# Performance work log

Measured on AMD Instinct MI355X. Metric: run time of the kernel, lower is better.

Reference implementation:

```python
import jax, jax.numpy as jnp
import numpy as np

K = 1024  # number of superpixel ids (matches fill_max of superpixel)

@jax.custom_vjp
def smooth_square(x):
    return x * x

def _ss_fwd(x):
    return x * x, x

def _ss_bwd(x, g):
    # gradient of square with input clipped to [-1, 1]
    return (g * 2.0 * jnp.clip(x, -1.0, 1.0),)

smooth_square.defvjp(_ss_fwd, _ss_bwd)

def setup_inputs() -> dict:
    key = jax.random.key(0)
    k1, k2 = jax.random.split(key)
    D, H, W = 64, 1024, 1024
    embedding = jax.random.normal(k1, (D, H, W), dtype=jnp.float32)
    superpixel = jax.random.randint(k2, (H, W), 0, K, dtype=jnp.int64)
    return {"embedding": embedding, "superpixel": superpixel}

def reference(embedding, superpixel):
    # embedding: D x H x W float, superpixel: H x W int
    D = embedding.shape[0]
    sp = superpixel.reshape(-1)                      # N = H*W
    x = embedding.reshape(D, -1)                     # D x N
    ones = jnp.ones(sp.shape, dtype=x.dtype)
    counts = jax.ops.segment_sum(ones, sp, num_segments=K)        # K
    sums = jax.ops.segment_sum(x.T, sp, num_segments=K)           # K x D
    mean = sums / jnp.maximum(counts, 1.0)[:, None]                # K x D
    dev = x - mean[sp].T                              # D x N, scores - per-segment mean
    # sum over all segments of D*variance*count == sum of squared deviations
    return smooth_square(dev).sum()
```

## Files before the change

kernel.cpp:

```cpp
#include <hip/hip_runtime.h>
#include <stdint.h>

#define K_SEG 1024
#define D_CH 64
#define CHUNK 32768
#define ABLK 512
#define PREP_B 128


__global__ void __launch_bounds__(256)
prep_kernel(const int* __restrict__ spw, uint16_t* __restrict__ sp16,
            uint32_t* __restrict__ cnt_part, float* __restrict__ sums,
            uint32_t* __restrict__ ticket, int N) {
    __shared__ uint32_t h[4][K_SEG];
    __shared__ int wideflag;
    const int t = threadIdx.x;
    const int b = blockIdx.x;
    {
        uint32_t* hf = &h[0][0];
        for (int i = t; i < 4 * K_SEG; i += 256) hf[i] = 0u;
    }
    if (t < 64) {
        int odd = spw[2 * t + 1];
        unsigned long long bal = __ballot(odd == 0);
        if (t == 0) wideflag = (bal == ~0ULL) ? 1 : 0;
    }
    if (b == 0 && t == 0) *ticket = 0u;
    if (b < D_CH)
        for (int i = t; i < K_SEG; i += 256) sums[b * K_SEG + i] = 0.0f;
    __syncthreads();
    const bool wide = (wideflag != 0);
    uint32_t* ht = h[t >> 6];
    const int stride = PREP_B * 256;
    #pragma unroll 4
    for (int n = b * 256 + t; n < N; n += stride) {
        int v = wide ? spw[2 * n] : spw[n];
        v &= (K_SEG - 1);
        sp16[n] = (uint16_t)v;
        ht[v] += 1u;
    }
    __syncthreads();
    for (int k = t; k < K_SEG; k += 256)
        cnt_part[b * K_SEG + k] = h[0][k] + h[1][k] + h[2][k] + h[3][k];
}

__global__ void __launch_bounds__(ABLK, 8)
accum_kernel(const float* __restrict__ emb, const uint16_t* __restrict__ sp16,
             float* __restrict__ sums, double* __restrict__ xsq_part, int N) {
    __shared__ float2 lsum[4][K_SEG];
    __shared__ float wsum[8];
    const int t = threadIdx.x;
    float2* tile = lsum[(t >> 6) & 3];
    {
        float2* lf = &lsum[0][0];
        for (int i = t; i < 4 * K_SEG; i += ABLK) lf[i] = make_float2(0.0f, 0.0f);
    }
    __syncthreads();

    const int g = blockIdx.x;
    const int c = blockIdx.y;
    const int base = c * CHUNK;
    const float* e0 = emb + (size_t)(2 * g) * N + base;
    const float* e1 = e0 + N;
    const uint16_t* sp = sp16 + base;
    float acc = 0.0f;
    const int NIT = CHUNK / (ABLK * 4);

    if (base + CHUNK <= N) {
        int q = t * 4;
        ushort4 k4 = *reinterpret_cast<const ushort4*>(sp + q);
        float4 v0 = *reinterpret_cast<const float4*>(e0 + q);
        float4 v1 = *reinterpret_cast<const float4*>(e1 + q);
        #pragma unroll 2
        for (int it = 0; it < NIT; ++it) {
            const int qn = q + ABLK * 4;
            ushort4 k4n = k4; float4 v0n = v0, v1n = v1;
            if (it + 1 < NIT) {
                k4n = *reinterpret_cast<const ushort4*>(sp + qn);
                v0n = *reinterpret_cast<const float4*>(e0 + qn);
                v1n = *reinterpret_cast<const float4*>(e1 + qn);
            }
            acc += v0.x * v0.x + v0.y * v0.y + v0.z * v0.z + v0.w * v0.w;
            acc += v1.x * v1.x + v1.y * v1.y + v1.z * v1.z + v1.w * v1.w;
            float2 o;
            o = tile[k4.x]; o.x += v0.x; o.y += v1.x; tile[k4.x] = o;
            o = tile[k4.y]; o.x += v0.y; o.y += v1.y; tile[k4.y] = o;
            o = tile[k4.z]; o.x += v0.z; o.y += v1.z; tile[k4.z] = o;
            o = tile[k4.w]; o.x += v0.w; o.y += v1.w; tile[k4.w] = o;
            q = qn; k4 = k4n; v0 = v0n; v1 = v1n;
        }
    } else {
        for (int it = 0; it < NIT; ++it) {
            const int p = base + it * ABLK * 4 + t * 4;
            if (p + 4 <= N) {
                const ushort4 k4 = *reinterpret_cast<const ushort4*>(sp16 + p);
                const float4 v0 = *reinterpret_cast<const float4*>(emb + (size_t)(2 * g) * N + p);
                const float4 v1 = *reinterpret_cast<const float4*>(emb + (size_t)(2 * g + 1) * N + p);
                acc += v0.x * v0.x + v0.y * v0.y + v0.z * v0.z + v0.w * v0.w;
                acc += v1.x * v1.x + v1.y * v1.y + v1.z * v1.z + v1.w * v1.w;
                float2 o;
                o = tile[k4.x]; o.x += v0.x; o.y += v1.x; tile[k4.x] = o;
                o = tile[k4.y]; o.x += v0.y; o.y += v1.y; tile[k4.y] = o;
                o = tile[k4.z]; o.x += v0.z; o.y += v1.z; tile[k4.z] = o;
                o = tile[k4.w]; o.x += v0.w; o.y += v1.w; tile[k4.w] = o;
            }
        }
    }
    __syncthreads();

    for (int k = t; k < K_SEG; k += ABLK) {
        float2 s0 = lsum[0][k], s1 = lsum[1][k], s2 = lsum[2][k], s3 = lsum[3][k];
        atomicAdd(&sums[(size_t)(2 * g) * K_SEG + k], s0.x + s1.x + s2.x + s3.x);
        atomicAdd(&sums[(size_t)(2 * g + 1) * K_SEG + k], s0.y + s1.y + s2.y + s3.y);
    }

    #pragma unroll
    for (int off = 32; off; off >>= 1) acc += __shfl_down(acc, off, 64);
    if ((t & 63) == 0) wsum[t >> 6] = acc;
    __syncthreads();
    if (t == 0) {
        double bsum = 0.0;
        #pragma unroll
        for (int w = 0; w < 8; ++w) bsum += (double)wsum[w];
        xsq_part[c * gridDim.x + g] = bsum;
    }
}

__global__ void __launch_bounds__(256)
finalize_kernel(const float* __restrict__ sums, const uint32_t* __restrict__ cnt_part,
                const double* __restrict__ xsq_part, double* __restrict__ term_part,
                uint32_t* __restrict__ ticket, float* __restrict__ out,
                int n_xsq) {
    const int t = threadIdx.x;
    const int b = blockIdx.x;
    const int k0 = b * 16;
    __shared__ float cinv[16];
    if (t < 16) {
        uint32_t c = 0;
        #pragma unroll 8
        for (int p = 0; p < PREP_B; ++p) c += cnt_part[p * K_SEG + k0 + t];
        cinv[t] = 1.0f / fmaxf((float)c, 1.0f);
    }
    __syncthreads();
    double acc = 0.0;
    for (int e = t; e < D_CH * 16; e += 256) {
        const int d = e >> 4, kk = e & 15;
        const float s = sums[d * K_SEG + k0 + kk];
        acc += (double)(s * s) * (double)cinv[kk];
    }
    __shared__ double sacc[256];
    sacc[t] = acc;
    __syncthreads();
    for (int off = 128; off; off >>= 1) {
        if (t < off) sacc[t] += sacc[t + off];
        __syncthreads();
    }
    __shared__ int last;
    if (t == 0) {
        term_part[b] = sacc[0];
        __threadfence();
        last = (atomicAdd(ticket, 1u) == gridDim.x - 1) ? 1 : 0;
    }
    __syncthreads();
    if (last) {
        double a = 0.0;
        for (int i = t; i < n_xsq; i += 256) a += xsq_part[i];
        if (t < 64) a -= atomicAdd(&term_part[t], 0.0);
        sacc[t] = a;
        __syncthreads();
        for (int off = 128; off; off >>= 1) {
            if (t < off) sacc[t] += sacc[t + off];
            __syncthreads();
        }
        if (t == 0) out[0] = (float)sacc[0];
    }
}

extern "C" void kernel_launch(void* const* d_in, const int* in_sizes, int n_in,
                              void* d_out, int out_size, void* d_ws, size_t ws_size,
                              hipStream_t stream) {
    const float* emb = (const float*)d_in[0];
    const int* spw = (const int*)d_in[1];
    const int N = in_sizes[1];

    char* ws = (char*)d_ws;
    uint32_t* ticket = (uint32_t*)(ws + 0);
    double* term_part = (double*)(ws + 64);
    double* xsq_part = (double*)(ws + 1024);
    float* sums = (float*)(ws + 16384);
    uint32_t* cnt_part = (uint32_t*)(ws + 278528);
    uint16_t* sp16 = (uint16_t*)(ws + 802816);

    prep_kernel<<<PREP_B, 256, 0, stream>>>(spw, sp16, cnt_part, sums, ticket, N);

    dim3 grid(D_CH / 2, (N + CHUNK - 1) / CHUNK);
    accum_kernel<<<grid, ABLK, 0, stream>>>(emb, sp16, sums, xsq_part, N);

    const int n_xsq = grid.x * grid.y;
    finalize_kernel<<<64, 256, 0, stream>>>(sums, cnt_part, xsq_part, term_part,
                                            ticket, (float*)d_out, n_xsq);
}
```

Measured before the change: 68.61 us.

## Replace global atomic segment sums with per-chunk partials and vectorized prep

When workspace allows, accum blocks write per-chunk partial sums to distinct slots instead of issuing global atomicAdds. A finalize kernel then reduces those partials over chunks per (d,k). The count reduction and reciprocal move into the g==0 accum blocks, and prep now uses 256 blocks of 512 threads with int4 loads and ushort4 stores. Atomic contention goes away, at the cost of extra partial-buffer traffic (32x64x1024 floats) and a serial chunk loop in finalize.

```diff
diff --git a/kernel.cpp b/kernel.cpp
--- a/kernel.cpp
+++ b/kernel.cpp
@@ -5,20 +5,22 @@
 #define D_CH 64
 #define CHUNK 32768
 #define ABLK 512
-#define PREP_B 128
-
-
-__global__ void __launch_bounds__(256)
-prep_kernel(const int* __restrict__ spw, uint16_t* __restrict__ sp16,
-            uint32_t* __restrict__ cnt_part, float* __restrict__ sums,
-            uint32_t* __restrict__ ticket, int N) {
-    __shared__ uint32_t h[4][K_SEG];
+#define NPREP_A 256
+#define TPREP_A 512
+#define NPREP_B 128
+#define TPREP_B 256
+
+
+__global__ void prep_kernel(const int* __restrict__ spw, uint16_t* __restrict__ sp16,
+                            uint32_t* __restrict__ cnt_part, float* __restrict__ sums,
+                            uint32_t* __restrict__ ticket, int N, int zero_sums) {
+    __shared__ uint32_t h[8][K_SEG];
     __shared__ int wideflag;
-    const int t = threadIdx.x;
-    const int b = blockIdx.x;
+    const int t = threadIdx.x, b = blockIdx.x;
+    const int tpb = blockDim.x, nw = tpb >> 6;
     {
         uint32_t* hf = &h[0][0];
-        for (int i = t; i < 4 * K_SEG; i += 256) hf[i] = 0u;
+        for (int i = t; i < nw * K_SEG; i += tpb) hf[i] = 0u;
     }
     if (t < 64) {
         int odd = spw[2 * t + 1];
@@ -26,29 +28,47 @@
         if (t == 0) wideflag = (bal == ~0ULL) ? 1 : 0;
     }
     if (b == 0 && t == 0) *ticket = 0u;
-    if (b < D_CH)
-        for (int i = t; i < K_SEG; i += 256) sums[b * K_SEG + i] = 0.0f;
+    if (zero_sums) {
+        for (int i = t; i < (D_CH * K_SEG) / NPREP_B; i += tpb)
+            sums[b * ((D_CH * K_SEG) / NPREP_B) + i] = 0.0f;
+    }
     __syncthreads();
     const bool wide = (wideflag != 0);
     uint32_t* ht = h[t >> 6];
-    const int stride = PREP_B * 256;
-    #pragma unroll 4
-    for (int n = b * 256 + t; n < N; n += stride) {
-        int v = wide ? spw[2 * n] : spw[n];
-        v &= (K_SEG - 1);
-        sp16[n] = (uint16_t)v;
-        ht[v] += 1u;
-    }
-    __syncthreads();
-    for (int k = t; k < K_SEG; k += 256)
-        cnt_part[b * K_SEG + k] = h[0][k] + h[1][k] + h[2][k] + h[3][k];
-}
-
+    const int step = gridDim.x * tpb * 4;
+    for (int n0 = (b * tpb + t) * 4; n0 + 4 <= N; n0 += step) {
+        int i0, i1, i2, i3;
+        if (wide) {
+            int4 a = *reinterpret_cast<const int4*>(spw + 2 * (size_t)n0);
+            int4 c = *reinterpret_cast<const int4*>(spw + 2 * (size_t)n0 + 4);
+            i0 = a.x; i1 = a.z; i2 = c.x; i3 = c.z;
+        } else {
+            int4 a = *reinterpret_cast<const int4*>(spw + n0);
+            i0 = a.x; i1 = a.y; i2 = a.z; i3 = a.w;
+        }
+        i0 &= K_SEG - 1; i1 &= K_SEG - 1; i2 &= K_SEG - 1; i3 &= K_SEG - 1;
+        ushort4 s4;
+        s4.x = (uint16_t)i0; s4.y = (uint16_t)i1; s4.z = (uint16_t)i2; s4.w = (uint16_t)i3;
+        *reinterpret_cast<ushort4*>(sp16 + n0) = s4;
+        ht[i0]++; ht[i1]++; ht[i2]++; ht[i3]++;
+    }
+    __syncthreads();
+    for (int k = t; k < K_SEG; k += tpb) {
+        uint32_t c = 0;
+        for (int w = 0; w < nw; ++w) c += h[w][k];
+        cnt_part[(size_t)b * K_SEG + k] = c;
+    }
+}
+
+template <bool PARTIALS>
 __global__ void __launch_bounds__(ABLK, 8)
 accum_kernel(const float* __restrict__ emb, const uint16_t* __restrict__ sp16,
-             float* __restrict__ sums, double* __restrict__ xsq_part, int N) {
+             float* __restrict__ outp, float* __restrict__ cinv,
+             const uint32_t* __restrict__ cnt_part, double* __restrict__ xsq_part,
+             int N, int nchunks) {
     __shared__ float2 lsum[4][K_SEG];
     __shared__ float wsum[8];
+    __shared__ int lastdummy;  (void)lastdummy;
     const int t = threadIdx.x;
     float2* tile = lsum[(t >> 6) & 3];
     {
@@ -82,11 +102,18 @@
             }
             acc += v0.x * v0.x + v0.y * v0.y + v0.z * v0.z + v0.w * v0.w;
             acc += v1.x * v1.x + v1.y * v1.y + v1.z * v1.z + v1.w * v1.w;
-            float2 o;
-            o = tile[k4.x]; o.x += v0.x; o.y += v1.x; tile[k4.x] = o;
-            o = tile[k4.y]; o.x += v0.y; o.y += v1.y; tile[k4.y] = o;
-            o = tile[k4.z]; o.x += v0.z; o.y += v1.z; tile[k4.z] = o;
-            o = tile[k4.w]; o.x += v0.w; o.y += v1.w; tile[k4.w] = o;
+            float2 o0 = tile[k4.x];
+            float2 o1 = tile[k4.y];
+            float2 o2 = tile[k4.z];
+            float2 o3 = tile[k4.w];
+            o0.x += v0.x; o0.y += v1.x;
+            o1.x += v0.y; o1.y += v1.y;
+            o2.x += v0.z; o2.y += v1.z;
+            o3.x += v0.w; o3.y += v1.w;
+            tile[k4.x] = o0;
+            tile[k4.y] = o1;
+            tile[k4.z] = o2;
+            tile[k4.w] = o3;
             q = qn; k4 = k4n; v0 = v0n; v1 = v1n;
         }
     } else {
@@ -98,20 +125,29 @@
                 const float4 v1 = *reinterpret_cast<const float4*>(emb + (size_t)(2 * g + 1) * N + p);
                 acc += v0.x * v0.x + v0.y * v0.y + v0.z * v0.z + v0.w * v0.w;
                 acc += v1.x * v1.x + v1.y * v1.y + v1.z * v1.z + v1.w * v1.w;
-                float2 o;
-                o = tile[k4.x]; o.x += v0.x; o.y += v1.x; tile[k4.x] = o;
-                o = tile[k4.y]; o.x += v0.y; o.y += v1.y; tile[k4.y] = o;
-                o = tile[k4.z]; o.x += v0.z; o.y += v1.z; tile[k4.z] = o;
-                o = tile[k4.w]; o.x += v0.w; o.y += v1.w; tile[k4.w] = o;
+                float2 o0 = tile[k4.x], o1 = tile[k4.y], o2 = tile[k4.z], o3 = tile[k4.w];
+                o0.x += v0.x; o0.y += v1.x;
+                o1.x += v0.y; o1.y += v1.y;
+                o2.x += v0.z; o2.y += v1.z;
+                o3.x += v0.w; o3.y += v1.w;
+                tile[k4.x] = o0; tile[k4.y] = o1; tile[k4.z] = o2; tile[k4.w] = o3;
             }
         }
     }
     __syncthreads();
 
+    const size_t baseA = ((size_t)c * D_CH + 2 * g) * K_SEG;
     for (int k = t; k < K_SEG; k += ABLK) {
         float2 s0 = lsum[0][k], s1 = lsum[1][k], s2 = lsum[2][k], s3 = lsum[3][k];
-        atomicAdd(&sums[(size_t)(2 * g) * K_SEG + k], s0.x + s1.x + s2.x + s3.x);
-        atomicAdd(&sums[(size_t)(2 * g + 1) * K_SEG + k], s0.y + s1.y + s2.y + s3.y);
+        float sx = s0.x + s1.x + s2.x + s3.x;
+        float sy = s0.y + s1.y + s2.y + s3.y;
+        if (PARTIALS) {
+            outp[baseA + k] = sx;
+            outp[baseA + K_SEG + k] = sy;
+        } else {
+            atomicAdd(&outp[(size_t)(2 * g) * K_SEG + k], sx);
+            atomicAdd(&outp[(size_t)(2 * g + 1) * K_SEG + k], sy);
+        }
     }
 
     #pragma unroll
@@ -124,30 +160,41 @@
         for (int w = 0; w < 8; ++w) bsum += (double)wsum[w];
         xsq_part[c * gridDim.x + g] = bsum;
     }
+
+    if (PARTIALS && g == 0) {
+        __syncthreads();
+        uint32_t* sc = reinterpret_cast<uint32_t*>(&lsum[0][0]);
+        for (int kbase = c * 32; kbase < K_SEG; kbase += 32 * nchunks) {
+            const int kk = kbase + (t & 31);
+            uint32_t s = 0;
+            const int j0 = (t >> 5) * (NPREP_A / 16);
+            for (int j = j0; j < j0 + NPREP_A / 16; ++j)
+                s += cnt_part[(size_t)j * K_SEG + kk];
+            sc[(t >> 5) * 32 + (t & 31)] = s;
+            __syncthreads();
+            if (t < 32) {
+                uint32_t ctot = 0;
+                #pragma unroll
+                for (int sl = 0; sl < 16; ++sl) ctot += sc[sl * 32 + t];
+                cinv[kbase + t] = 1.0f / fmaxf((float)ctot, 1.0f);
+            }
+            __syncthreads();
+        }
+    }
 }
 
 __global__ void __launch_bounds__(256)
-finalize_kernel(const float* __restrict__ sums, const uint32_t* __restrict__ cnt_part,
-                const double* __restrict__ xsq_part, double* __restrict__ term_part,
-                uint32_t* __restrict__ ticket, float* __restrict__ out,
-                int n_xsq) {
-    const int t = threadIdx.x;
-    const int b = blockIdx.x;
-    const int k0 = b * 16;
-    __shared__ float cinv[16];
-    if (t < 16) {
-        uint32_t c = 0;
-        #pragma unroll 8
-        for (int p = 0; p < PREP_B; ++p) c += cnt_part[p * K_SEG + k0 + t];
-        cinv[t] = 1.0f / fmaxf((float)c, 1.0f);
-    }
-    __syncthreads();
-    double acc = 0.0;
-    for (int e = t; e < D_CH * 16; e += 256) {
-        const int d = e >> 4, kk = e & 15;
-        const float s = sums[d * K_SEG + k0 + kk];
-        acc += (double)(s * s) * (double)cinv[kk];
-    }
+finalizeA_kernel(const float* __restrict__ part, const float* __restrict__ cinv,
+                 double* __restrict__ xsq_part, double* __restrict__ term_part,
+                 uint32_t* __restrict__ ticket, float* __restrict__ out,
+                 int nchunks, int n_xsq) {
+    const int t = threadIdx.x, b = blockIdx.x;
+    const int d = b >> 2;
+    const int k = (b & 3) * 256 + t;
+    float S = 0.0f;
+    for (int c = 0; c < nchunks; ++c)
+        S += part[((size_t)c * D_CH + d) * K_SEG + k];
+    double acc = (double)S * (double)S * (double)cinv[k];
     __shared__ double sacc[256];
     sacc[t] = acc;
     __syncthreads();
@@ -164,7 +211,55 @@
     __syncthreads();
     if (last) {
         double a = 0.0;
-        for (int i = t; i < n_xsq; i += 256) a += xsq_part[i];
+        for (int i = t; i < n_xsq; i += 256) a += atomicAdd(&xsq_part[i], 0.0);
+        a -= atomicAdd(&term_part[t], 0.0);
+        sacc[t] = a;
+        __syncthreads();
+        for (int off = 128; off; off >>= 1) {
+            if (t < off) sacc[t] += sacc[t + off];
+            __syncthreads();
+        }
+        if (t == 0) out[0] = (float)sacc[0];
+    }
+}
+
+__global__ void __launch_bounds__(256)
+finalizeB_kernel(const float* __restrict__ sums, const uint32_t* __restrict__ cnt_part,
+                 double* __restrict__ xsq_part, double* __restrict__ term_part,
+                 uint32_t* __restrict__ ticket, float* __restrict__ out, int n_xsq) {
+    const int t = threadIdx.x, b = blockIdx.x;
+    const int k0 = b * 16;
+    __shared__ float cinv16[16];
+    if (t < 16) {
+        uint32_t c = 0;
+        #pragma unroll 8
+        for (int p = 0; p < NPREP_B; ++p) c += cnt_part[p * K_SEG + k0 + t];
+        cinv16[t] = 1.0f / fmaxf((float)c, 1.0f);
+    }
+    __syncthreads();
+    double acc = 0.0;
+    for (int e = t; e < D_CH * 16; e += 256) {
+        const int d = e >> 4, kk = e & 15;
+        const float s = sums[d * K_SEG + k0 + kk];
+        acc += (double)(s * s) * (double)cinv16[kk];
+    }
+    __shared__ double sacc[256];
+    sacc[t] = acc;
+    __syncthreads();
+    for (int off = 128; off; off >>= 1) {
+        if (t < off) sacc[t] += sacc[t + off];
+        __syncthreads();
+    }
+    __shared__ int last;
+    if (t == 0) {
+        term_part[b] = sacc[0];
+        __threadfence();
+        last = (atomicAdd(ticket, 1u) == gridDim.x - 1) ? 1 : 0;
+    }
+    __syncthreads();
+    if (last) {
+        double a = 0.0;
+        for (int i = t; i < n_xsq; i += 256) a += atomicAdd(&xsq_part[i], 0.0);
         if (t < 64) a -= atomicAdd(&term_part[t], 0.0);
         sacc[t] = a;
         __syncthreads();
@@ -182,21 +277,42 @@
     const float* emb = (const float*)d_in[0];
     const int* spw = (const int*)d_in[1];
     const int N = in_sizes[1];
+    const int nchunks = (N + CHUNK - 1) / CHUNK;
 
     char* ws = (char*)d_ws;
     uint32_t* ticket = (uint32_t*)(ws + 0);
     double* term_part = (double*)(ws + 64);
-    double* xsq_part = (double*)(ws + 1024);
-    float* sums = (float*)(ws + 16384);
-    uint32_t* cnt_part = (uint32_t*)(ws + 278528);
-    uint16_t* sp16 = (uint16_t*)(ws + 802816);
-
-    prep_kernel<<<PREP_B, 256, 0, stream>>>(spw, sp16, cnt_part, sums, ticket, N);
-
-    dim3 grid(D_CH / 2, (N + CHUNK - 1) / CHUNK);
-    accum_kernel<<<grid, ABLK, 0, stream>>>(emb, sp16, sums, xsq_part, N);
-
-    const int n_xsq = grid.x * grid.y;
-    finalize_kernel<<<64, 256, 0, stream>>>(sums, cnt_part, xsq_part, term_part,
-                                            ticket, (float*)d_out, n_xsq);
-}
+    double* xsq_part = (double*)(ws + 4096);
+    float* cinv = (float*)(ws + 12288);
+    uint32_t* cnt_part = (uint32_t*)(ws + 16384);
+
+    const size_t partA_off = 16384 + (size_t)NPREP_A * K_SEG * 4;
+    const size_t sp16A_off = partA_off + (size_t)32 * D_CH * K_SEG * 4;
+    const size_t needA = sp16A_off + 2 * (size_t)N;
+    const bool big = (ws_size >= needA) && (nchunks <= 32) && (N % 4 == 0);
+
+    dim3 agrid(D_CH / 2, nchunks);
+    const int n_xsq = agrid.x * agrid.y;
+
+    if (big) {
+        float* part = (float*)(ws + partA_off);
+        uint16_t* sp16 = (uint16_t*)(ws + sp16A_off);
+        prep_kernel<<<NPREP_A, TPREP_A, 0, stream>>>(spw, sp16, cnt_part, nullptr,
+                                                     ticket, N, 0);
+        accum_kernel<true><<<agrid, ABLK, 0, stream>>>(emb, sp16, part, cinv,
+                                                       cnt_part, xsq_part, N, nchunks);
+        finalizeA_kernel<<<256, 256, 0, stream>>>(part, cinv, xsq_part, term_part,
+                                                  ticket, (float*)d_out, nchunks, n_xsq);
+    } else {
+        const size_t sumsB_off = 16384 + (size_t)NPREP_B * K_SEG * 4;
+        const size_t sp16B_off = sumsB_off + (size_t)D_CH * K_SEG * 4;
+        float* sums = (float*)(ws + sumsB_off);
+        uint16_t* sp16 = (uint16_t*)(ws + sp16B_off);
+        prep_kernel<<<NPREP_B, TPREP_B, 0, stream>>>(spw, sp16, cnt_part, sums,
+                                                     ticket, N, 1);
+        accum_kernel<false><<<agrid, ABLK, 0, stream>>>(emb, sp16, sums, cinv,
+                                                        cnt_part, xsq_part, N, nchunks);
+        finalizeB_kernel<<<64, 256, 0, stream>>>(sums, cnt_part, xsq_part, term_part,
+                                                 ticket, (float*)d_out, n_xsq);
+    }
+}
```

Result: slower. 72.53 us (+5.7%).

## Process four channels per block with float4 LDS tiles and split global sums

Applied to the files above, without the earlier changes.

Each accum block now handles four embedding channels instead of two, so each segment-id load and each LDS read-modify-write is shared across four channels using float4 tiles. The LDS copies drop from four per-wavefront float2 tiles to two half-block float4 tiles, and CHUNK is halved so the grid keeps enough blocks. Global sums are split into two buffers by chunk parity to reduce atomic contention, and finalize adds the two buffers together. The trade-off is more LDS bank conflicts between wavefronts that now share a tile, plus higher register pressure from the extra prefetched float4 values.

```diff
diff --git a/kernel.cpp b/kernel.cpp
--- a/kernel.cpp
+++ b/kernel.cpp
@@ -3,7 +3,7 @@
 
 #define K_SEG 1024
 #define D_CH 64
-#define CHUNK 32768
+#define CHUNK 16384
 #define ABLK 512
 #define PREP_B 128
 
@@ -26,8 +26,8 @@
         if (t == 0) wideflag = (bal == ~0ULL) ? 1 : 0;
     }
     if (b == 0 && t == 0) *ticket = 0u;
-    if (b < D_CH)
-        for (int i = t; i < K_SEG; i += 256) sums[b * K_SEG + i] = 0.0f;
+    for (int i = t; i < (2 * D_CH * K_SEG) / PREP_B; i += 256)
+        sums[b * ((2 * D_CH * K_SEG) / PREP_B) + i] = 0.0f;
     __syncthreads();
     const bool wide = (wideflag != 0);
     uint32_t* ht = h[t >> 6];
@@ -47,21 +47,22 @@
 __global__ void __launch_bounds__(ABLK, 8)
 accum_kernel(const float* __restrict__ emb, const uint16_t* __restrict__ sp16,
              float* __restrict__ sums, double* __restrict__ xsq_part, int N) {
-    __shared__ float2 lsum[4][K_SEG];
+    __shared__ float4 lsum[2][K_SEG];
     __shared__ float wsum[8];
     const int t = threadIdx.x;
-    float2* tile = lsum[(t >> 6) & 3];
+    float4* tile = lsum[t >> 8];
     {
-        float2* lf = &lsum[0][0];
-        for (int i = t; i < 4 * K_SEG; i += ABLK) lf[i] = make_float2(0.0f, 0.0f);
+        float4* lf = &lsum[0][0];
+        for (int i = t; i < 2 * K_SEG; i += ABLK)
+            lf[i] = make_float4(0.0f, 0.0f, 0.0f, 0.0f);
     }
     __syncthreads();
 
     const int g = blockIdx.x;
     const int c = blockIdx.y;
     const int base = c * CHUNK;
-    const float* e0 = emb + (size_t)(2 * g) * N + base;
-    const float* e1 = e0 + N;
+    const float* e0 = emb + (size_t)(4 * g) * N + base;
+    const size_t sN = (size_t)N;
     const uint16_t* sp = sp16 + base;
     float acc = 0.0f;
     const int NIT = CHUNK / (ABLK * 4);
@@ -70,48 +71,61 @@
         int q = t * 4;
         ushort4 k4 = *reinterpret_cast<const ushort4*>(sp + q);
         float4 v0 = *reinterpret_cast<const float4*>(e0 + q);
-        float4 v1 = *reinterpret_cast<const float4*>(e1 + q);
+        float4 v1 = *reinterpret_cast<const float4*>(e0 + sN + q);
+        float4 v2 = *reinterpret_cast<const float4*>(e0 + 2 * sN + q);
+        float4 v3 = *reinterpret_cast<const float4*>(e0 + 3 * sN + q);
         #pragma unroll 2
         for (int it = 0; it < NIT; ++it) {
             const int qn = q + ABLK * 4;
-            ushort4 k4n = k4; float4 v0n = v0, v1n = v1;
+            ushort4 k4n = k4; float4 v0n = v0, v1n = v1, v2n = v2, v3n = v3;
             if (it + 1 < NIT) {
                 k4n = *reinterpret_cast<const ushort4*>(sp + qn);
                 v0n = *reinterpret_cast<const float4*>(e0 + qn);
-                v1n = *reinterpret_cast<const float4*>(e1 + qn);
+                v1n = *reinterpret_cast<const float4*>(e0 + sN + qn);
+                v2n = *reinterpret_cast<const float4*>(e0 + 2 * sN + qn);
+                v3n = *reinterpret_cast<const float4*>(e0 + 3 * sN + qn);
             }
             acc += v0.x * v0.x + v0.y * v0.y + v0.z * v0.z + v0.w * v0.w;
             acc += v1.x * v1.x + v1.y * v1.y + v1.z * v1.z + v1.w * v1.w;
-            float2 o;
-            o = tile[k4.x]; o.x += v0.x; o.y += v1.x; tile[k4.x] = o;
-            o = tile[k4.y]; o.x += v0.y; o.y += v1.y; tile[k4.y] = o;
-            o = tile[k4.z]; o.x += v0.z; o.y += v1.z; tile[k4.z] = o;
-            o = tile[k4.w]; o.x += v0.w; o.y += v1.w; tile[k4.w] = o;
-            q = qn; k4 = k4n; v0 = v0n; v1 = v1n;
+            acc += v2.x * v2.x + v2.y * v2.y + v2.z * v2.z + v2.w * v2.w;
+            acc += v3.x * v3.x + v3.y * v3.y + v3.z * v3.z + v3.w * v3.w;
+            float4 o;
+            o = tile[k4.x]; o.x += v0.x; o.y += v1.x; o.z += v2.x; o.w += v3.x; tile[k4.x] = o;
+            o = tile[k4.y]; o.x += v0.y; o.y += v1.y; o.z += v2.y; o.w += v3.y; tile[k4.y] = o;
+            o = tile[k4.z]; o.x += v0.z; o.y += v1.z; o.z += v2.z; o.w += v3.z; tile[k4.z] = o;
+            o = tile[k4.w]; o.x += v0.w; o.y += v1.w; o.z += v2.w; o.w += v3.w; tile[k4.w] = o;
+            q = qn; k4 = k4n; v0 = v0n; v1 = v1n; v2 = v2n; v3 = v3n;
         }
     } else {
         for (int it = 0; it < NIT; ++it) {
             const int p = base + it * ABLK * 4 + t * 4;
             if (p + 4 <= N) {
                 const ushort4 k4 = *reinterpret_cast<const ushort4*>(sp16 + p);
-                const float4 v0 = *reinterpret_cast<const float4*>(emb + (size_t)(2 * g) * N + p);
-                const float4 v1 = *reinterpret_cast<const float4*>(emb + (size_t)(2 * g + 1) * N + p);
+                const float4 v0 = *reinterpret_cast<const float4*>(emb + (size_t)(4 * g) * N + p);
+                const float4 v1 = *reinterpret_cast<const float4*>(emb + (size_t)(4 * g + 1) * N + p);
+                const float4 v2 = *reinterpret_cast<const float4*>(emb + (size_t)(4 * g + 2) * N + p);
+                const float4 v3 = *reinterpret_cast<const float4*>(emb + (size_t)(4 * g + 3) * N + p);
                 acc += v0.x * v0.x + v0.y * v0.y + v0.z * v0.z + v0.w * v0.w;
                 acc += v1.x * v1.x + v1.y * v1.y + v1.z * v1.z + v1.w * v1.w;
-                float2 o;
-                o = tile[k4.x]; o.x += v0.x; o.y += v1.x; tile[k4.x] = o;
-                o = tile[k4.y]; o.x += v0.y; o.y += v1.y; tile[k4.y] = o;
-                o = tile[k4.z]; o.x += v0.z; o.y += v1.z; tile[k4.z] = o;
-                o = tile[k4.w]; o.x += v0.w; o.y += v1.w; tile[k4.w] = o;
+                acc += v2.x * v2.x + v2.y * v2.y + v2.z * v2.z + v2.w * v2.w;
+                acc += v3.x * v3.x + v3.y * v3.y + v3.z * v3.z + v3.w * v3.w;
+                float4 o;
+                o = tile[k4.x]; o.x += v0.x; o.y += v1.x; o.z += v2.x; o.w += v3.x; tile[k4.x] = o;
+                o = tile[k4.y]; o.x += v0.y; o.y += v1.y; o.z += v2.y; o.w += v3.y; tile[k4.y] = o;
+                o = tile[k4.z]; o.x += v0.z; o.y += v1.z; o.z += v2.z; o.w += v3.z; tile[k4.z] = o;
+                o = tile[k4.w]; o.x += v0.w; o.y += v1.w; o.z += v2.w; o.w += v3.w; tile[k4.w] = o;
             }
         }
     }
     __syncthreads();
 
+    float* dst = sums + (size_t)(c & 1) * (D_CH * K_SEG);
     for (int k = t; k < K_SEG; k += ABLK) {
-        float2 s0 = lsum[0][k], s1 = lsum[1][k], s2 = lsum[2][k], s3 = lsum[3][k];
-        atomicAdd(&sums[(size_t)(2 * g) * K_SEG + k], s0.x + s1.x + s2.x + s3.x);
-        atomicAdd(&sums[(size_t)(2 * g + 1) * K_SEG + k], s0.y + s1.y + s2.y + s3.y);
+        float4 s0 = lsum[0][k], s1 = lsum[1][k];
+        atomicAdd(&dst[(size_t)(4 * g + 0) * K_SEG + k], s0.x + s1.x);
+        atomicAdd(&dst[(size_t)(4 * g + 1) * K_SEG + k], s0.y + s1.y);
+        atomicAdd(&dst[(size_t)(4 * g + 2) * K_SEG + k], s0.z + s1.z);
+        atomicAdd(&dst[(size_t)(4 * g + 3) * K_SEG + k], s0.w + s1.w);
     }
 
     #pragma unroll
@@ -128,25 +142,24 @@
 
 __global__ void __launch_bounds__(256)
 finalize_kernel(const float* __restrict__ sums, const uint32_t* __restrict__ cnt_part,
-                const double* __restrict__ xsq_part, double* __restrict__ term_part,
-                uint32_t* __restrict__ ticket, float* __restrict__ out,
-                int n_xsq) {
-    const int t = threadIdx.x;
-    const int b = blockIdx.x;
+                double* __restrict__ xsq_part, double* __restrict__ term_part,
+                uint32_t* __restrict__ ticket, float* __restrict__ out, int n_xsq) {
+    const int t = threadIdx.x, b = blockIdx.x;
     const int k0 = b * 16;
-    __shared__ float cinv[16];
+    __shared__ float cinv16[16];
     if (t < 16) {
         uint32_t c = 0;
         #pragma unroll 8
         for (int p = 0; p < PREP_B; ++p) c += cnt_part[p * K_SEG + k0 + t];
-        cinv[t] = 1.0f / fmaxf((float)c, 1.0f);
+        cinv16[t] = 1.0f / fmaxf((float)c, 1.0f);
     }
     __syncthreads();
     double acc = 0.0;
     for (int e = t; e < D_CH * 16; e += 256) {
         const int d = e >> 4, kk = e & 15;
-        const float s = sums[d * K_SEG + k0 + kk];
-        acc += (double)(s * s) * (double)cinv[kk];
+        const float s = sums[d * K_SEG + k0 + kk] +
+                        sums[D_CH * K_SEG + d * K_SEG + k0 + kk];
+        acc += (double)(s * s) * (double)cinv16[kk];
     }
     __shared__ double sacc[256];
     sacc[t] = acc;
@@ -186,17 +199,17 @@
     char* ws = (char*)d_ws;
     uint32_t* ticket = (uint32_t*)(ws + 0);
     double* term_part = (double*)(ws + 64);
-    double* xsq_part = (double*)(ws + 1024);
-    float* sums = (float*)(ws + 16384);
-    uint32_t* cnt_part = (uint32_t*)(ws + 278528);
-    uint16_t* sp16 = (uint16_t*)(ws + 802816);
+    double* xsq_part = (double*)(ws + 4096);
+    uint32_t* cnt_part = (uint32_t*)(ws + 16384);
+    float* sums = (float*)(ws + 540672);
+    uint16_t* sp16 = (uint16_t*)(ws + 1064960);
 
     prep_kernel<<<PREP_B, 256, 0, stream>>>(spw, sp16, cnt_part, sums, ticket, N);
 
-    dim3 grid(D_CH / 2, (N + CHUNK - 1) / CHUNK);
-    accum_kernel<<<grid, ABLK, 0, stream>>>(emb, sp16, sums, xsq_part, N);
-
-    const int n_xsq = grid.x * grid.y;
+    dim3 agrid(D_CH / 4, (N + CHUNK - 1) / CHUNK);
+    accum_kernel<<<agrid, ABLK, 0, stream>>>(emb, sp16, sums, xsq_part, N);
+
+    const int n_xsq = agrid.x * agrid.y;
     finalize_kernel<<<64, 256, 0, stream>>>(sums, cnt_part, xsq_part, term_part,
                                             ticket, (float*)d_out, n_xsq);
 }
```

Measured after the change: 93.46 us. 36.2% more time.
